# Kernel optimization log

Measured on AMD Instinct MI355X. Metric: run time of the kernel, lower is better.

The kernel has to match this reference:

```python
import jax, jax.numpy as jnp
import numpy as np

B, IN, OUT = 131072, 256, 256
BITWIDTH = 7.0


def setup_inputs() -> dict:
    key = jax.random.key(0)
    k1, k2 = jax.random.split(key)
    # simulated int8 activations (integer-valued float32)
    act_in = jax.random.randint(k1, (B, IN), -127, 128).astype(jnp.float32)
    # UniformWeights: xavier_uniform then weight_quant to the int8 grid
    limit = float(np.sqrt(6.0 / (IN + OUT)))
    w = jax.random.uniform(k2, (OUT, IN), minval=-limit, maxval=limit, dtype=jnp.float32)
    w_range = jnp.max(jnp.abs(w))
    weight_exp = (jnp.ceil(jnp.log2(w_range)) - 7.0).astype(jnp.int32)
    weight = jnp.round(w / w_range * 127.0)  # int8-valued float32 [OUT, IN]
    return {"act_in": act_in, "exp_in": jnp.int32(0), "weight": weight, "weight_exp": weight_exp}


def _round_shift(x, shift):
    # RoundShift: floor-div by 2**shift, add floor(|remainder| / 2**(shift-1)), clip to int8
    two_s = jnp.exp2(shift)
    rt = jnp.floor(x / two_s)
    prob = jnp.abs(x - rt * two_s)
    dec = jnp.floor(prob / jnp.exp2(shift - 1.0))
    return jnp.clip(rt + dec, -127.0, 127.0)


def reference(act_in, exp_in, weight, weight_exp):
    # int8 GEMM simulated in fp32 (exact: |acc| < 2^24)
    temp = act_in @ weight.T  # [B, OUT] int32 accumulator values
    # RangeEstimate: full-tensor abs-max -> bitwidth
    r = jnp.max(jnp.abs(temp))
    bw = jnp.where(r > 0, jnp.ceil(jnp.log2(jnp.maximum(r, 1.0))), 0.0)
    shift = bw - BITWIDTH
    pos = shift > 0
    safe_shift = jnp.maximum(shift, 1.0)
    rounded = _round_shift(temp, safe_shift)
    act_out = jnp.where(pos, rounded, temp).astype(jnp.int8)
    exp_sum = jnp.asarray(exp_in, jnp.int32) + jnp.asarray(weight_exp, jnp.int32)
    exp_out = (exp_sum + jnp.where(pos, shift, 0.0).astype(jnp.int32)).astype(jnp.int16)
    return act_out, exp_out
```

## Files before the change

### kernel.cpp

```cpp
#include <hip/hip_runtime.h>
#include <stdint.h>


#define M_ROWS 131072
#define NK 256
#define BM 32
#define AKP 264

typedef __attribute__((ext_vector_type(8))) short bf16x8;
typedef __attribute__((ext_vector_type(4))) float f32x4;
typedef __attribute__((ext_vector_type(4))) float fv4;
typedef __attribute__((ext_vector_type(4))) int iv4;
typedef __attribute__((ext_vector_type(4))) unsigned int u32x4;
typedef __attribute__((ext_vector_type(4))) unsigned short us4;

__device__ __forceinline__ uint32_t pack_bf16(float a, float b) {
  return (__float_as_uint(a) >> 16) | (__float_as_uint(b) & 0xFFFF0000u);
}

__global__ void wconv(const float* __restrict__ w, unsigned short* __restrict__ wb) {
  const int i = blockIdx.x * 256 + threadIdx.x;
  const fv4 f = ((const fv4*)w)[i];
  us4 o;
  o.x = (unsigned short)(__float_as_uint(f.x) >> 16);
  o.y = (unsigned short)(__float_as_uint(f.y) >> 16);
  o.z = (unsigned short)(__float_as_uint(f.z) >> 16);
  o.w = (unsigned short)(__float_as_uint(f.w) >> 16);
  ((us4*)wb)[i] = o;
}

__global__ __launch_bounds__(256) void gemm_store_max(
    const float* __restrict__ act,
    const unsigned short* __restrict__ wgtb,
    int* __restrict__ temp,
    int* __restrict__ gmax)
{
  __shared__ __align__(16) short As[BM * AKP];
  __shared__ int smax;

  const int tid = threadIdx.x;
  if (tid == 0) smax = 0;

  const int bm   = blockIdx.x * BM;
  const int lane = tid & 63;
  const int wave = tid >> 6;
  const int lm   = lane & 15;
  const int lk   = lane >> 4;
  const int wn   = wave * 64;

  const int arow = tid >> 5;
  const int aseg = tid & 31;
  const float* pbase = act + (size_t)(bm + arow) * NK + aseg * 8;
  fv4 fr[8];
#pragma unroll
  for (int j = 0; j < 4; ++j) {
    const float* p = pbase + (size_t)(j * 8) * NK;
    fr[2 * j]     = *(const fv4*)p;
    fr[2 * j + 1] = *((const fv4*)p + 1);
  }

  const unsigned short* bbase = wgtb + (size_t)(wn + lm) * NK + lk * 8;
  bf16x8 bcur[4];
#pragma unroll
  for (int ni = 0; ni < 4; ++ni)
    bcur[ni] = *(const bf16x8*)(bbase + (size_t)(ni * 16) * NK);

#pragma unroll
  for (int j = 0; j < 4; ++j) {
    uint32_t pk[4];
    pk[0] = pack_bf16(fr[2 * j].x, fr[2 * j].y);
    pk[1] = pack_bf16(fr[2 * j].z, fr[2 * j].w);
    pk[2] = pack_bf16(fr[2 * j + 1].x, fr[2 * j + 1].y);
    pk[3] = pack_bf16(fr[2 * j + 1].z, fr[2 * j + 1].w);
    *(u32x4*)&As[(arow + j * 8) * AKP + aseg * 8] = *(const u32x4*)pk;
  }
  __syncthreads();

  f32x4 acc[2][4] = {};

#pragma unroll
  for (int k8 = 0; k8 < 8; ++k8) {
    bf16x8 bnxt[4];
    if (k8 < 7) {
      const int kkn = (k8 + 1) * 32;
#pragma unroll
      for (int ni = 0; ni < 4; ++ni)
        bnxt[ni] = *(const bf16x8*)(bbase + (size_t)(ni * 16) * NK + kkn);
    }
    const int kk = k8 * 32;
    bf16x8 af[2];
#pragma unroll
    for (int mi = 0; mi < 2; ++mi)
      af[mi] = *(const bf16x8*)&As[(mi * 16 + lm) * AKP + kk + lk * 8];
#pragma unroll
    for (int mi = 0; mi < 2; ++mi)
#pragma unroll
      for (int ni = 0; ni < 4; ++ni)
        acc[mi][ni] = __builtin_amdgcn_mfma_f32_16x16x32_bf16(
            bcur[ni], af[mi], acc[mi][ni], 0, 0, 0);
    if (k8 < 7) {
#pragma unroll
      for (int ni = 0; ni < 4; ++ni) bcur[ni] = bnxt[ni];
    }
  }

  int imax = 0;
#pragma unroll
  for (int mi = 0; mi < 2; ++mi) {
    const size_t rowoff = (size_t)(bm + mi * 16 + lm) * NK;
#pragma unroll
    for (int ni = 0; ni < 4; ++ni) {
      iv4 qv;
#pragma unroll
      for (int r = 0; r < 4; ++r) {
        const int iv = (int)acc[mi][ni][r];
        qv[r] = iv;
        const int a = iv < 0 ? -iv : iv;
        imax = a > imax ? a : imax;
      }
      *(iv4*)&temp[rowoff + wn + ni * 16 + lk * 4] = qv;
    }
  }
#pragma unroll
  for (int off = 32; off; off >>= 1) {
    const int o = __shfl_xor(imax, off, 64);
    imax = o > imax ? o : imax;
  }
  if (lane == 0) atomicMax(&smax, imax);
  __syncthreads();
  if (tid == 0) atomicMax(gmax, smax);
}

__global__ __launch_bounds__(256) void quant_stream(
    const int* __restrict__ temp, int* __restrict__ out,
    const int* __restrict__ gmax,
    const int* __restrict__ exp_in, const int* __restrict__ wexp)
{
  const int r = *gmax;
  const int bw = (r <= 1) ? 0 : (32 - __clz(r - 1));
  const int shift = bw - 7;
  const bool pos = shift > 0;
  const int s = shift < 1 ? 1 : shift;

  const int base = blockIdx.x * 1024 + threadIdx.x;
  const iv4* pin = (const iv4*)temp;
  iv4* pout = (iv4*)out;

  iv4 v[4];
#pragma unroll
  for (int j = 0; j < 4; ++j) v[j] = pin[base + j * 256];

#pragma unroll
  for (int j = 0; j < 4; ++j) {
    iv4 o;
#pragma unroll
    for (int e = 0; e < 4; ++e) {
      const int ti = v[j][e];
      int q;
      if (pos) {
        const int rt = ti >> s;
        const int dec = (ti - (rt << s)) >> (s - 1);
        q = rt + dec;
        q = q > 127 ? 127 : (q < -127 ? -127 : q);
      } else {
        q = (int)(signed char)(ti & 0xFF);
      }
      o[e] = q;
    }
    __builtin_nontemporal_store(o, &pout[base + j * 256]);
  }

  if (base == 0) {
    const int e = exp_in[0] + wexp[0] + (pos ? shift : 0);
    out[(size_t)M_ROWS * NK] = (int)(short)e;
  }
}

extern "C" void kernel_launch(void* const* d_in, const int* in_sizes, int n_in,
                              void* d_out, int out_size, void* d_ws, size_t ws_size,
                              hipStream_t stream) {
  const float* act   = (const float*)d_in[0];
  const int* exp_in  = (const int*)d_in[1];
  const float* wgt   = (const float*)d_in[2];
  const int* wexp    = (const int*)d_in[3];

  int* gmax          = (int*)d_ws;
  unsigned short* wb = (unsigned short*)((char*)d_ws + 4096);
  int* temp          = (int*)((char*)d_ws + (1 << 20));

  (void)hipMemsetAsync(d_ws, 0, sizeof(int), stream);
  wconv<<<dim3(64), dim3(256), 0, stream>>>(wgt, wb);
  gemm_store_max<<<dim3(M_ROWS / BM), dim3(256), 0, stream>>>(act, wb, temp, gmax);
  quant_stream<<<dim3(8192), dim3(256), 0, stream>>>(temp, (int*)d_out, gmax,
                                                     exp_in, wexp);
}
```

Baseline: 316.9 us.

## Stage weight half in LDS and load activations directly into MFMA registers

The GEMM kernel now runs 512 blocks of 1024 threads. Each block loads half of the pre-swizzled bf16 weight matrix (64 KB) into LDS with global_load_lds, then each wave streams its own activation rows from global memory straight into registers and converts them to bf16 MFMA fragments. This removes the per-block activation LDS staging and the repeated global weight fetches, and wconv rewrites the weights into a k-blocked layout to suit the LDS reads. The costs are 64 KB of LDS per block, which limits occupancy, less coalesced activation loads, and two column-half blocks each reading the same activation rows.

```diff
diff --git a/kernel.cpp b/kernel.cpp
--- a/kernel.cpp
+++ b/kernel.cpp
@@ -4,14 +4,11 @@
 
 #define M_ROWS 131072
 #define NK 256
-#define BM 32
-#define AKP 264
 
 typedef __attribute__((ext_vector_type(8))) short bf16x8;
 typedef __attribute__((ext_vector_type(4))) float f32x4;
 typedef __attribute__((ext_vector_type(4))) float fv4;
 typedef __attribute__((ext_vector_type(4))) int iv4;
-typedef __attribute__((ext_vector_type(4))) unsigned int u32x4;
 typedef __attribute__((ext_vector_type(4))) unsigned short us4;
 
 __device__ __forceinline__ uint32_t pack_bf16(float a, float b) {
@@ -20,115 +17,102 @@
 
 __global__ void wconv(const float* __restrict__ w, unsigned short* __restrict__ wb) {
   const int i = blockIdx.x * 256 + threadIdx.x;
+  const int n = i >> 6;
+  const int k = (i & 63) * 4;
   const fv4 f = ((const fv4*)w)[i];
   us4 o;
   o.x = (unsigned short)(__float_as_uint(f.x) >> 16);
   o.y = (unsigned short)(__float_as_uint(f.y) >> 16);
   o.z = (unsigned short)(__float_as_uint(f.z) >> 16);
   o.w = (unsigned short)(__float_as_uint(f.w) >> 16);
-  ((us4*)wb)[i] = o;
+  *(us4*)&wb[(k >> 5) * 8192 + n * 32 + (k & 31)] = o;
 }
 
-__global__ __launch_bounds__(256) void gemm_store_max(
+__global__ __launch_bounds__(1024, 4) void gemm_store_max(
     const float* __restrict__ act,
     const unsigned short* __restrict__ wgtb,
     int* __restrict__ temp,
     int* __restrict__ gmax)
 {
-  __shared__ __align__(16) short As[BM * AKP];
-  __shared__ int smax;
+  extern __shared__ __align__(16) char lds_raw[];
+  short* Bs = (short*)lds_raw;
 
-  const int tid = threadIdx.x;
-  if (tid == 0) smax = 0;
-
-  const int bm   = blockIdx.x * BM;
+  const int tid  = threadIdx.x;
+  const int wave = tid >> 6;
   const int lane = tid & 63;
-  const int wave = tid >> 6;
-  const int lm   = lane & 15;
-  const int lk   = lane >> 4;
-  const int wn   = wave * 64;
-
-  const int arow = tid >> 5;
-  const int aseg = tid & 31;
-  const float* pbase = act + (size_t)(bm + arow) * NK + aseg * 8;
-  fv4 fr[8];
-#pragma unroll
-  for (int j = 0; j < 4; ++j) {
-    const float* p = pbase + (size_t)(j * 8) * NK;
-    fr[2 * j]     = *(const fv4*)p;
-    fr[2 * j + 1] = *((const fv4*)p + 1);
-  }
-
-  const unsigned short* bbase = wgtb + (size_t)(wn + lm) * NK + lk * 8;
-  bf16x8 bcur[4];
-#pragma unroll
-  for (int ni = 0; ni < 4; ++ni)
-    bcur[ni] = *(const bf16x8*)(bbase + (size_t)(ni * 16) * NK);
+  const int l15  = lane & 15;
+  const int lq   = lane >> 4;
+  const int h    = blockIdx.x & 1;
+  const int g    = blockIdx.x >> 1;
 
 #pragma unroll
   for (int j = 0; j < 4; ++j) {
-    uint32_t pk[4];
-    pk[0] = pack_bf16(fr[2 * j].x, fr[2 * j].y);
-    pk[1] = pack_bf16(fr[2 * j].z, fr[2 * j].w);
-    pk[2] = pack_bf16(fr[2 * j + 1].x, fr[2 * j + 1].y);
-    pk[3] = pack_bf16(fr[2 * j + 1].z, fr[2 * j + 1].w);
-    *(u32x4*)&As[(arow + j * 8) * AKP + aseg * 8] = *(const u32x4*)pk;
+    const int seg = wave * 4 + j;
+    const char* gsrc = (const char*)wgtb + (seg >> 3) * 16384 + h * 8192 +
+                       (seg & 7) * 1024 + lane * 16;
+    char* ldst = lds_raw + seg * 1024 + lane * 16;
+    __builtin_amdgcn_global_load_lds(
+        (const __attribute__((address_space(1))) unsigned int*)gsrc,
+        (__attribute__((address_space(3))) unsigned int*)ldst, 16, 0, 0);
   }
   __syncthreads();
 
-  f32x4 acc[2][4] = {};
+  int imax = 0;
 
 #pragma unroll
-  for (int k8 = 0; k8 < 8; ++k8) {
-    bf16x8 bnxt[4];
-    if (k8 < 7) {
-      const int kkn = (k8 + 1) * 32;
+  for (int s = 0; s < 2; ++s) {
+    const int m0 = g * 512 + wave * 32 + s * 16;
+    const float* ap = act + (size_t)(m0 + l15) * NK + lq * 8;
+
+    fv4 a0[8], a1[8];
 #pragma unroll
-      for (int ni = 0; ni < 4; ++ni)
-        bnxt[ni] = *(const bf16x8*)(bbase + (size_t)(ni * 16) * NK + kkn);
+    for (int k8 = 0; k8 < 8; ++k8) {
+      a0[k8] = *(const fv4*)(ap + k8 * 32);
+      a1[k8] = *(const fv4*)(ap + k8 * 32 + 4);
     }
-    const int kk = k8 * 32;
-    bf16x8 af[2];
+    bf16x8 af[8];
 #pragma unroll
-    for (int mi = 0; mi < 2; ++mi)
-      af[mi] = *(const bf16x8*)&As[(mi * 16 + lm) * AKP + kk + lk * 8];
+    for (int k8 = 0; k8 < 8; ++k8) {
+      uint32_t pk[4];
+      pk[0] = pack_bf16(a0[k8].x, a0[k8].y);
+      pk[1] = pack_bf16(a0[k8].z, a0[k8].w);
+      pk[2] = pack_bf16(a1[k8].x, a1[k8].y);
+      pk[3] = pack_bf16(a1[k8].z, a1[k8].w);
+      af[k8] = *(const bf16x8*)pk;
+    }
+
+    f32x4 acc[8] = {};
 #pragma unroll
-    for (int mi = 0; mi < 2; ++mi)
+    for (int k8 = 0; k8 < 8; ++k8) {
+      const int cbase = k8 * 4096 + l15 * 32 + lq * 8;
 #pragma unroll
-      for (int ni = 0; ni < 4; ++ni)
-        acc[mi][ni] = __builtin_amdgcn_mfma_f32_16x16x32_bf16(
-            bcur[ni], af[mi], acc[mi][ni], 0, 0, 0);
-    if (k8 < 7) {
+      for (int ni = 0; ni < 8; ++ni) {
+        const bf16x8 bfr = *(const bf16x8*)&Bs[cbase + ni * 512];
+        acc[ni] = __builtin_amdgcn_mfma_f32_16x16x32_bf16(bfr, af[k8], acc[ni], 0, 0, 0);
+      }
+    }
+
+    int* orow = temp + (size_t)(m0 + l15) * NK + h * 128 + lq * 4;
 #pragma unroll
-      for (int ni = 0; ni < 4; ++ni) bcur[ni] = bnxt[ni];
-    }
-  }
-
-  int imax = 0;
-#pragma unroll
-  for (int mi = 0; mi < 2; ++mi) {
-    const size_t rowoff = (size_t)(bm + mi * 16 + lm) * NK;
-#pragma unroll
-    for (int ni = 0; ni < 4; ++ni) {
+    for (int ni = 0; ni < 8; ++ni) {
       iv4 qv;
 #pragma unroll
       for (int r = 0; r < 4; ++r) {
-        const int iv = (int)acc[mi][ni][r];
+        const int iv = (int)acc[ni][r];
         qv[r] = iv;
         const int a = iv < 0 ? -iv : iv;
         imax = a > imax ? a : imax;
       }
-      *(iv4*)&temp[rowoff + wn + ni * 16 + lk * 4] = qv;
+      *(iv4*)&orow[ni * 16] = qv;
     }
   }
+
 #pragma unroll
   for (int off = 32; off; off >>= 1) {
     const int o = __shfl_xor(imax, off, 64);
     imax = o > imax ? o : imax;
   }
-  if (lane == 0) atomicMax(&smax, imax);
-  __syncthreads();
-  if (tid == 0) atomicMax(gmax, smax);
+  if (lane == 0) atomicMax(gmax, imax);
 }
 
 __global__ __launch_bounds__(256) void quant_stream(
@@ -190,7 +174,7 @@
 
   (void)hipMemsetAsync(d_ws, 0, sizeof(int), stream);
   wconv<<<dim3(64), dim3(256), 0, stream>>>(wgt, wb);
-  gemm_store_max<<<dim3(M_ROWS / BM), dim3(256), 0, stream>>>(act, wb, temp, gmax);
+  gemm_store_max<<<dim3(512), dim3(1024), 65536, stream>>>(act, wb, temp, gmax);
   quant_stream<<<dim3(8192), dim3(256), 0, stream>>>(temp, (int*)d_out, gmax,
                                                      exp_in, wexp);
 }
```

Measured after the change: 347.4 us. 9.6% more time.
